# Kernel tuning notes

Measured on AMD Instinct MI355X. Metric: run time of the kernel, lower is better.

## Reference

```python
import jax, jax.numpy as jnp
import numpy as np

G = 64        # graphs per batch
N = 256       # nodes per graph (= num omics modalities)
O = 256       # omics modalities
D_IN = 128    # per-omics input dim
H = 64        # hidden_dim
HEADS = 4
E_PER = 8192  # edges per graph (avg degree 32)
NUM_NODES = G * N
E = G * E_PER
BN_EPS = 1e-5


def setup_inputs() -> dict:
    key = jax.random.key(0)
    ks = jax.random.split(key, 24)
    f = jax.random.normal
    # per-graph random edges, offset into the batched node space
    src = jax.random.randint(ks[0], (G, E_PER), 0, N)
    dst = jax.random.randint(ks[1], (G, E_PER), 0, N)
    off = (jnp.arange(G) * N)[:, None]
    edge_index = jnp.stack([(src + off).reshape(-1), (dst + off).reshape(-1)]).astype(jnp.int64)
    batch_ids = jnp.repeat(jnp.arange(G), N).astype(jnp.int64)
    return {
        "omics": f(ks[2], (G, O, D_IN), jnp.float32),
        "w_omics": f(ks[3], (O, D_IN, H), jnp.float32) * 0.05,
        "b_omics": f(ks[4], (O, H), jnp.float32) * 0.05,
        "rot": f(ks[5], (O, H), jnp.float32),
        "bn_gamma": jnp.ones((O, H), jnp.float32),
        "bn_beta": jnp.zeros((O, H), jnp.float32),
        "bn_mean": f(ks[6], (O, H), jnp.float32) * 0.1,
        "bn_var": jax.random.uniform(ks[7], (O, H), jnp.float32, 0.5, 1.5),
        "gat1_w": f(ks[8], (H, HEADS * H), jnp.float32) * 0.05,
        "att_src1": f(ks[9], (HEADS, H), jnp.float32) * 0.05,
        "att_dst1": f(ks[10], (HEADS, H), jnp.float32) * 0.05,
        "bias1": jnp.zeros((HEADS * H,), jnp.float32),
        "gat2_w": f(ks[11], (HEADS * H, H), jnp.float32) * 0.05,
        "att_src2": f(ks[12], (1, H), jnp.float32) * 0.05,
        "att_dst2": f(ks[13], (1, H), jnp.float32) * 0.05,
        "bias2": jnp.zeros((H,), jnp.float32),
        "cls_w1": f(ks[14], (H, H), jnp.float32) * 0.05,
        "cls_b1": jnp.zeros((H,), jnp.float32),
        "cls_w2": f(ks[15], (H, 1), jnp.float32) * 0.05,
        "cls_b2": jnp.zeros((1,), jnp.float32),
        "edge_index": edge_index,
        "batch_ids": batch_ids,
    }


def _gat(x, src, dst, W, a_src, a_dst, bias, heads, c):
    # PyG GATConv: linear -> per-edge attention logits -> segment softmax over dst -> scatter-sum
    h = (x @ W).reshape(-1, heads, c)                       # [NUM_NODES, heads, c]
    a_s = jnp.sum(h * a_src, axis=-1)                       # [NUM_NODES, heads]
    a_d = jnp.sum(h * a_dst, axis=-1)
    logit = jax.nn.leaky_relu(a_s[src] + a_d[dst], 0.2)     # [E, heads]
    m = jax.ops.segment_max(logit, dst, num_segments=NUM_NODES)
    m = jnp.where(jnp.isfinite(m), m, 0.0)                  # nodes with no in-edges
    e = jnp.exp(logit - m[dst])
    s = jax.ops.segment_sum(e, dst, num_segments=NUM_NODES)
    alpha = e / (s[dst] + 1e-16)                            # [E, heads]
    msg = h[src] * alpha[..., None]                         # [E, heads, c] (dominant traffic)
    out = jax.ops.segment_sum(msg, dst, num_segments=NUM_NODES)
    return out.reshape(NUM_NODES, heads * c) + bias


def reference(omics, w_omics, b_omics, rot, bn_gamma, bn_beta, bn_mean, bn_var,
              gat1_w, att_src1, att_dst1, bias1, gat2_w, att_src2, att_dst2, bias2,
              cls_w1, cls_b1, cls_w2, cls_b2, edge_index, batch_ids):
    # quantum-inspired omics encoders (vectorized over the O modalities)
    h = jnp.einsum('bod,odh->boh', omics, w_omics) + b_omics
    h = jax.nn.relu(h * (jnp.cos(rot) + jnp.sin(rot)))
    h = (h - bn_mean) / jnp.sqrt(bn_var + BN_EPS) * bn_gamma + bn_beta  # BatchNorm eval mode
    x = h.reshape(NUM_NODES, H)

    src, dst = edge_index[0], edge_index[1]
    x = jax.nn.elu(_gat(x, src, dst, gat1_w, att_src1, att_dst1, bias1, HEADS, H))
    x = _gat(x, src, dst, gat2_w, att_src2, att_dst2, bias2, 1, H)

    pooled = jax.ops.segment_sum(x, batch_ids, num_segments=G) / N  # global_mean_pool
    z = jax.nn.relu(pooled @ cls_w1 + cls_b1)
    out = jax.nn.sigmoid(z @ cls_w2 + cls_b2)
    return out, pooled
```

## Files before the change

### kernel.cpp

```cpp
#include <hip/hip_runtime.h>
#include <hip/hip_bf16.h>
#include <math.h>

#define G 64
#define NNODE 256
#define D_IN 128
#define HDIM 64
#define HEADS 4
#define E_PER 8192
#define NUM_NODES (G * NNODE)
#define E_TOTAL (G * E_PER)
#define BN_EPS 1e-5f

typedef __attribute__((ext_vector_type(8))) short bf16x8;
typedef __attribute__((ext_vector_type(4))) float f32x4;

__device__ __forceinline__ float lrelu02(float x) { return x > 0.f ? x : 0.2f * x; }
__device__ __forceinline__ unsigned short f2bf(float f) {
    unsigned u = __float_as_uint(f);
    return (unsigned short)((u + 0x7FFFu + ((u >> 16) & 1u)) >> 16);
}
__device__ __forceinline__ unsigned long long pk4(float a, float b, float c, float d) {
    return (unsigned long long)f2bf(a)
         | ((unsigned long long)f2bf(b) << 16)
         | ((unsigned long long)f2bf(c) << 32)
         | ((unsigned long long)f2bf(d) << 48);
}

__global__ __launch_bounds__(512) void setup_kernel(
    const int* __restrict__ eidx, unsigned int* __restrict__ cntm,
    const float* __restrict__ omics, const float* __restrict__ w,
    const float* __restrict__ b, const float* __restrict__ rot,
    const float* __restrict__ gamma, const float* __restrict__ beta,
    const float* __restrict__ mean, const float* __restrict__ var,
    unsigned short* __restrict__ xb,
    const float* __restrict__ w1, const float* __restrict__ w2,
    unsigned short* __restrict__ wt1, unsigned short* __restrict__ wt2)
{
    __shared__ union {
        struct { float Wl[D_IN * HDIM]; float Om[G * 132]; } enc;
        unsigned cw[NNODE * 64];
    } sm;
    int blk = blockIdx.x;
    int t = threadIdx.x;

    if (blk < G) {
        int g = blk;
        float4 z4 = make_float4(0.f, 0.f, 0.f, 0.f);
        for (int i = t; i < 4096; i += 512) ((float4*)sm.cw)[i] = z4;
        __syncthreads();
        const int* srcp = eidx + (size_t)g * E_PER;
        const int* dstp = eidx + E_TOTAL + (size_t)g * E_PER;
        int base = g * NNODE;
        for (int e = t; e < E_PER; e += 512) {
            int s = srcp[e] - base, d = dstp[e] - base;
            atomicAdd(&sm.cw[(d << 6) + (s >> 2)], 1u << ((s & 3) * 8));
        }
        __syncthreads();
        for (int i = t; i < 4096; i += 512)
            ((float4*)(cntm + (size_t)g * 16384))[i] = ((const float4*)sm.cw)[i];
    } else if (blk < G + 256) {
        int o = blk - G;
        for (int i = t; i < D_IN * HDIM / 4; i += 512)
            ((float4*)sm.enc.Wl)[i] = ((const float4*)(w + (size_t)o * D_IN * HDIM))[i];
        for (int i = t; i < G * (D_IN / 4); i += 512) {
            int g = i >> 5, dq = i & 31;
            *((float4*)(sm.enc.Om + g * 132) + dq) =
                ((const float4*)(omics + ((size_t)g * NNODE + o) * D_IN))[dq];
        }
        __syncthreads();

        int cq = t & 15, gs = t >> 4;
        float4 acc[2];
        acc[0] = make_float4(0.f, 0.f, 0.f, 0.f);
        acc[1] = make_float4(0.f, 0.f, 0.f, 0.f);

        for (int d = 0; d < D_IN; ++d) {
            float4 wv = *(const float4*)&sm.enc.Wl[d * 64 + cq * 4];
            #pragma unroll
            for (int gi = 0; gi < 2; ++gi) {
                float ov = sm.enc.Om[(gi * 32 + gs) * 132 + d];
                acc[gi].x = fmaf(ov, wv.x, acc[gi].x);
                acc[gi].y = fmaf(ov, wv.y, acc[gi].y);
                acc[gi].z = fmaf(ov, wv.z, acc[gi].z);
                acc[gi].w = fmaf(ov, wv.w, acc[gi].w);
            }
        }

        float4 bv = ((const float4*)b)[o * 16 + cq];
        float4 rv = ((const float4*)rot)[o * 16 + cq];
        float4 mv = ((const float4*)mean)[o * 16 + cq];
        float4 vv = ((const float4*)var)[o * 16 + cq];
        float4 gv = ((const float4*)gamma)[o * 16 + cq];
        float4 be = ((const float4*)beta)[o * 16 + cq];
        float4 sc, kk;
        sc.x = cosf(rv.x) + sinf(rv.x); sc.y = cosf(rv.y) + sinf(rv.y);
        sc.z = cosf(rv.z) + sinf(rv.z); sc.w = cosf(rv.w) + sinf(rv.w);
        kk.x = gv.x * rsqrtf(vv.x + BN_EPS); kk.y = gv.y * rsqrtf(vv.y + BN_EPS);
        kk.z = gv.z * rsqrtf(vv.z + BN_EPS); kk.w = gv.w * rsqrtf(vv.w + BN_EPS);

        #pragma unroll
        for (int gi = 0; gi < 2; ++gi) {
            int g = gi * 32 + gs;
            float4 v;
            v.x = fmaxf((acc[gi].x + bv.x) * sc.x, 0.f);
            v.y = fmaxf((acc[gi].y + bv.y) * sc.y, 0.f);
            v.z = fmaxf((acc[gi].z + bv.z) * sc.z, 0.f);
            v.w = fmaxf((acc[gi].w + bv.w) * sc.w, 0.f);
            v.x = (v.x - mv.x) * kk.x + be.x;
            v.y = (v.y - mv.y) * kk.y + be.y;
            v.z = (v.z - mv.z) * kk.z + be.z;
            v.w = (v.w - mv.w) * kk.w + be.w;
            *(unsigned long long*)&xb[((size_t)(g * NNODE + o)) * 64 + cq * 4] =
                pk4(v.x, v.y, v.z, v.w);
        }
    } else {
        int pb = blk - (G + 256);
        int i0 = pb * 2048 + t;
        #pragma unroll
        for (int it = 0; it < 4; ++it) {
            int i = i0 + it * 512;
            int c = i >> 6, k = i & 63;
            wt1[c * 64 + k] = f2bf(w1[k * 256 + c]);
            int c2 = i >> 8, k2 = i & 255;
            wt2[c2 * 256 + k2] = f2bf(w2[k2 * 64 + c2]);
        }
    }
}

__global__ __launch_bounds__(512) void gat1_lin_mfma(
    const unsigned short* __restrict__ xb, const unsigned short* __restrict__ wt1,
    const float* __restrict__ att_s, const float* __restrict__ att_d,
    unsigned short* __restrict__ ht1, float* __restrict__ as1, float* __restrict__ ad1)
{
    int blk = blockIdx.x;
    int n0 = blk * 64;
    int g = n0 >> 8, soff = n0 & 255;
    __shared__ unsigned short Ab[64 * 64];
    __shared__ unsigned short Bb[256 * 64];
    int t = threadIdx.x;
    {
        int node = t >> 3, kg = t & 7;
        bf16x8 v = *(const bf16x8*)&xb[(size_t)(n0 + node) * 64 + kg * 8];
        *(bf16x8*)&Ab[node * 64 + ((kg ^ (node & 7)) << 3)] = v;
    }
    for (int i = t; i < 2048; i += 512) {
        int c = i >> 3, kg = i & 7;
        bf16x8 v = *(const bf16x8*)&wt1[c * 64 + kg * 8];
        *(bf16x8*)&Bb[c * 64 + ((kg ^ (c & 7)) << 3)] = v;
    }
    __syncthreads();

    int w = t >> 6, l = t & 63;
    int lrow = l & 15, lk = l >> 4;
    int mt = w >> 1, hh0 = (w & 1) * 2;
    int arow = mt * 16 + lrow;
    float asp[2][4], adp[2][4];
    #pragma unroll
    for (int hi = 0; hi < 2; ++hi)
        #pragma unroll
        for (int r = 0; r < 4; ++r) { asp[hi][r] = 0.f; adp[hi][r] = 0.f; }

    for (int ntl = 0; ntl < 8; ++ntl) {
        int nt = (w & 1) * 8 + ntl;
        int c = nt * 16 + lrow;
        f32x4 acc = {0.f, 0.f, 0.f, 0.f};
        #pragma unroll
        for (int kb = 0; kb < 2; ++kb) {
            int kg = kb * 4 + lk;
            bf16x8 a = *(const bf16x8*)&Ab[arow * 64 + ((kg ^ (arow & 7)) << 3)];
            bf16x8 b = *(const bf16x8*)&Bb[c * 64 + ((kg ^ (c & 7)) << 3)];
            acc = __builtin_amdgcn_mfma_f32_16x16x32_bf16(a, b, acc, 0, 0, 0);
        }
        int head = c >> 6, ch = c & 63;
        int sb = soff + mt * 16 + lk * 4;
        *(unsigned long long*)&ht1[(size_t)((g * HEADS + head) * 64 + ch) * 256 + sb] =
            pk4(acc[0], acc[1], acc[2], acc[3]);
        float av = att_s[c], dv = att_d[c];
        int hi = ntl >> 2;
        #pragma unroll
        for (int r = 0; r < 4; ++r) {
            asp[hi][r] = fmaf(acc[r], av, asp[hi][r]);
            adp[hi][r] = fmaf(acc[r], dv, adp[hi][r]);
        }
    }
    #pragma unroll
    for (int hi = 0; hi < 2; ++hi)
        #pragma unroll
        for (int r = 0; r < 4; ++r) {
            float a = asp[hi][r], d = adp[hi][r];
            a += __shfl_xor(a, 1); a += __shfl_xor(a, 2);
            a += __shfl_xor(a, 4); a += __shfl_xor(a, 8);
            d += __shfl_xor(d, 1); d += __shfl_xor(d, 2);
            d += __shfl_xor(d, 4); d += __shfl_xor(d, 8);
            if (lrow == 0) {
                int node = n0 + mt * 16 + lk * 4 + r;
                as1[node * HEADS + hh0 + hi] = a;
                ad1[node * HEADS + hh0 + hi] = d;
            }
        }
}

__global__ __launch_bounds__(512) void gat1_edge_mfma(
    const unsigned short* __restrict__ ht1, const float* __restrict__ as1,
    const float* __restrict__ ad1, const unsigned int* __restrict__ cntm,
    const float* __restrict__ bias1, unsigned short* __restrict__ x2b)
{
    int g = blockIdx.x, head = blockIdx.y, q = blockIdx.z;
    __shared__ unsigned short ht[64 * 256];
    __shared__ unsigned short Mb[64 * 256];
    __shared__ float asl[NNODE], adl[NNODE], u1[NNODE], u2[NNODE];
    __shared__ float v1[NNODE], v2[NNODE];
    __shared__ float wred[8];
    unsigned short* xs = Mb;
    int t = threadIdx.x;
    int r0 = q * 64;

    float va = -1e30f, vd = 0.f;
    if (t < NNODE) {
        va = as1[(g * NNODE + t) * HEADS + head];
        vd = ad1[(g * NNODE + t) * HEADS + head];
        asl[t] = va; adl[t] = vd;
    }
    {
        float mv = va;
        #pragma unroll
        for (int d = 32; d; d >>= 1) mv = fmaxf(mv, __shfl_xor(mv, d));
        if ((t & 63) == 0) wred[t >> 6] = mv;
    }
    __syncthreads();
    if (t < NNODE) {
        float M = fmaxf(fmaxf(wred[0], wred[1]), fmaxf(wred[2], wred[3]));
        float mt = lrelu02(M + vd);
        v1[t] = __expf(vd - mt);
        v2[t] = __expf(0.2f * vd - mt);
        u1[t] = __expf(va);
        u2[t] = __expf(0.2f * va);
    }
    for (int i = t; i < 2048; i += 512) {
        int c = i >> 5, sg = i & 31;
        bf16x8 v = *(const bf16x8*)&ht1[(size_t)((g * HEADS + head) * 64 + c) * 256 + sg * 8];
        *(bf16x8*)&ht[c * 256 + ((sg ^ (c & 31)) << 3)] = v;
    }
    __syncthreads();

    int w = t >> 6, l = t & 63;
    int lrow = l & 15, lk = l >> 4;
    int mt = w & 3, nb = (w >> 2) * 2;
    int ar = mt * 16 + lrow;
    int c0 = nb * 16 + lrow, c1 = c0 + 16;
    float b0v = bias1[head * 64 + c0], b1v = bias1[head * 64 + c1];
    const bf16x8 onev = {(short)0x3F80, (short)0x3F80, (short)0x3F80, (short)0x3F80,
                         (short)0x3F80, (short)0x3F80, (short)0x3F80, (short)0x3F80};

    for (int ri = w; ri < 64; ri += 8) {
        int d = r0 + ri;
        unsigned cwv = cntm[(((size_t)g * NNODE + d) << 6) + l];
        float adv = adl[d], vd1 = v1[d], vd2 = v2[d];
        float4 as4 = ((const float4*)asl)[l];
        float4 u14 = ((const float4*)u1)[l];
        float4 u24 = ((const float4*)u2)[l];
        float p0 = (float)(cwv & 0xFFu) *
                   ((as4.x + adv > 0.f) ? u14.x * vd1 : u24.x * vd2);
        float p1 = (float)((cwv >> 8) & 0xFFu) *
                   ((as4.y + adv > 0.f) ? u14.y * vd1 : u24.y * vd2);
        float p2 = (float)((cwv >> 16) & 0xFFu) *
                   ((as4.z + adv > 0.f) ? u14.z * vd1 : u24.z * vd2);
        float p3 = (float)(cwv >> 24) *
                   ((as4.w + adv > 0.f) ? u14.w * vd1 : u24.w * vd2);
        *(unsigned long long*)&Mb[ri * 256 + (((l >> 1) ^ (ri & 7)) << 3)
                                  + ((l & 1) << 2)] = pk4(p0, p1, p2, p3);
    }
    __syncthreads();

    f32x4 acc0 = {0.f, 0.f, 0.f, 0.f};
    f32x4 acc1 = {0.f, 0.f, 0.f, 0.f};
    f32x4 accd = {0.f, 0.f, 0.f, 0.f};
    #pragma unroll
    for (int kb = 0; kb < 8; ++kb) {
        int oct = kb * 4 + lk;
        bf16x8 a = *(const bf16x8*)&Mb[ar * 256 + ((oct ^ (ar & 7)) << 3)];
        bf16x8 b0 = *(const bf16x8*)&ht[c0 * 256 + ((oct ^ (c0 & 31)) << 3)];
        bf16x8 b1 = *(const bf16x8*)&ht[c1 * 256 + ((oct ^ (c1 & 31)) << 3)];
        accd = __builtin_amdgcn_mfma_f32_16x16x32_bf16(a, onev, accd, 0, 0, 0);
        acc0 = __builtin_amdgcn_mfma_f32_16x16x32_bf16(a, b0, acc0, 0, 0, 0);
        acc1 = __builtin_amdgcn_mfma_f32_16x16x32_bf16(a, b1, acc1, 0, 0, 0);
    }
    __syncthreads();
    #pragma unroll
    for (int r = 0; r < 4; ++r) {
        int rl = mt * 16 + lk * 4 + r;
        float inv = 1.f / (accd[r] + 1e-16f);
        float o0 = acc0[r] * inv + b0v;
        float o1 = acc1[r] * inv + b1v;
        o0 = o0 > 0.f ? o0 : expm1f(o0);
        o1 = o1 > 0.f ? o1 : expm1f(o1);
        xs[rl * 64 + c0] = f2bf(o0);
        xs[rl * 64 + c1] = f2bf(o1);
    }
    __syncthreads();
    {
        int row = t >> 3, cg = t & 7;
        bf16x8 v = *(const bf16x8*)&xs[row * 64 + cg * 8];
        *(bf16x8*)&x2b[(size_t)(g * NNODE + r0 + row) * 256 + head * 64 + cg * 8] = v;
    }
}

__global__ __launch_bounds__(512) void gat2_lin_mfma(
    const unsigned short* __restrict__ x2b, const unsigned short* __restrict__ wt2,
    const float* __restrict__ att_s, const float* __restrict__ att_d,
    unsigned short* __restrict__ ht2, float* __restrict__ as2, float* __restrict__ ad2)
{
    int blk = blockIdx.x;
    int n0 = blk * 64;
    int g = n0 >> 8, soff = n0 & 255;
    __shared__ unsigned short Ab[64 * 256];
    __shared__ unsigned short Bb[64 * 256];
    __shared__ float asr[64], adr[64];
    int t = threadIdx.x;
    for (int i = t; i < 2048; i += 512) {
        int node = i >> 5, kg = i & 31;
        bf16x8 v = *(const bf16x8*)&x2b[(size_t)(n0 + node) * 256 + kg * 8];
        *(bf16x8*)&Ab[node * 256 + ((kg ^ (node & 31)) << 3)] = v;
    }
    for (int i = t; i < 2048; i += 512) {
        int c = i >> 5, kg = i & 31;
        bf16x8 v = *(const bf16x8*)&wt2[c * 256 + kg * 8];
        *(bf16x8*)&Bb[c * 256 + ((kg ^ (c & 31)) << 3)] = v;
    }
    if (t < 64) { asr[t] = 0.f; adr[t] = 0.f; }
    __syncthreads();

    int w = t >> 6, l = t & 63;
    int lrow = l & 15, lk = l >> 4;
    int mt = w & 3, nb = (w >> 2) * 2;
    int ar = mt * 16 + lrow;
    float asp[2][4], adp[2][4];
    #pragma unroll
    for (int ni = 0; ni < 2; ++ni)
        #pragma unroll
        for (int r = 0; r < 4; ++r) { asp[ni][r] = 0.f; adp[ni][r] = 0.f; }

    #pragma unroll
    for (int ni = 0; ni < 2; ++ni) {
        int c = (nb + ni) * 16 + lrow;
        f32x4 acc = {0.f, 0.f, 0.f, 0.f};
        #pragma unroll
        for (int ks = 0; ks < 8; ++ks) {
            int kg = ks * 4 + lk;
            bf16x8 a = *(const bf16x8*)&Ab[ar * 256 + ((kg ^ (ar & 31)) << 3)];
            bf16x8 b = *(const bf16x8*)&Bb[c * 256 + ((kg ^ (c & 31)) << 3)];
            acc = __builtin_amdgcn_mfma_f32_16x16x32_bf16(a, b, acc, 0, 0, 0);
        }
        int sb = soff + mt * 16 + lk * 4;
        *(unsigned long long*)&ht2[(size_t)(g * 64 + c) * 256 + sb] =
            pk4(acc[0], acc[1], acc[2], acc[3]);
        float av = att_s[c], dv = att_d[c];
        #pragma unroll
        for (int r = 0; r < 4; ++r) {
            asp[ni][r] = fmaf(acc[r], av, asp[ni][r]);
            adp[ni][r] = fmaf(acc[r], dv, adp[ni][r]);
        }
    }
    #pragma unroll
    for (int ni = 0; ni < 2; ++ni)
        #pragma unroll
        for (int r = 0; r < 4; ++r) {
            float a = asp[ni][r], d = adp[ni][r];
            a += __shfl_xor(a, 1); a += __shfl_xor(a, 2);
            a += __shfl_xor(a, 4); a += __shfl_xor(a, 8);
            d += __shfl_xor(d, 1); d += __shfl_xor(d, 2);
            d += __shfl_xor(d, 4); d += __shfl_xor(d, 8);
            if (lrow == 0) {
                int rl = mt * 16 + lk * 4 + r;
                atomicAdd(&asr[rl], a);
                atomicAdd(&adr[rl], d);
            }
        }
    __syncthreads();
    if (t < 64) { as2[n0 + t] = asr[t]; ad2[n0 + t] = adr[t]; }
}

__global__ __launch_bounds__(512) void gat2_edge_mfma(
    const unsigned short* __restrict__ ht2, const float* __restrict__ as2,
    const float* __restrict__ ad2, const unsigned int* __restrict__ cntm,
    float* __restrict__ pl8)
{
    int g = blockIdx.x, by = blockIdx.y;
    __shared__ unsigned short ht[64 * 256];
    __shared__ unsigned short Mb[32 * 256];
    __shared__ float asl[NNODE], adl[NNODE], u1[NNODE], u2[NNODE];
    __shared__ float v1[NNODE], v2[NNODE];
    __shared__ float wred[8];
    __shared__ float pool[64];
    int t = threadIdx.x;

    float va = -1e30f, vd = 0.f;
    if (t < NNODE) {
        va = as2[g * NNODE + t];
        vd = ad2[g * NNODE + t];
        asl[t] = va; adl[t] = vd;
    }
    if (t < 64) pool[t] = 0.f;
    {
        float mv = va;
        #pragma unroll
        for (int d = 32; d; d >>= 1) mv = fmaxf(mv, __shfl_xor(mv, d));
        if ((t & 63) == 0) wred[t >> 6] = mv;
    }
    __syncthreads();
    if (t < NNODE) {
        float M = fmaxf(fmaxf(wred[0], wred[1]), fmaxf(wred[2], wred[3]));
        float mt = lrelu02(M + vd);
        v1[t] = __expf(vd - mt);
        v2[t] = __expf(0.2f * vd - mt);
        u1[t] = __expf(va);
        u2[t] = __expf(0.2f * va);
    }
    for (int i = t; i < 2048; i += 512) {
        int c = i >> 5, sg = i & 31;
        bf16x8 v = *(const bf16x8*)&ht2[(size_t)(g * 64 + c) * 256 + sg * 8];
        *(bf16x8*)&ht[c * 256 + ((sg ^ (c & 31)) << 3)] = v;
    }
    __syncthreads();

    int w = t >> 6, l = t & 63;
    int lrow = l & 15, lk = l >> 4;
    int r0 = by * 32;

    for (int ri = w; ri < 32; ri += 8) {
        int d = r0 + ri;
        unsigned cwv = cntm[(((size_t)g * NNODE + d) << 6) + l];
        float adv = adl[d], vd1 = v1[d], vd2 = v2[d];
        float4 as4 = ((const float4*)asl)[l];
        float4 u14 = ((const float4*)u1)[l];
        float4 u24 = ((const float4*)u2)[l];
        float p0 = (float)(cwv & 0xFFu) *
                   ((as4.x + adv > 0.f) ? u14.x * vd1 : u24.x * vd2);
        float p1 = (float)((cwv >> 8) & 0xFFu) *
                   ((as4.y + adv > 0.f) ? u14.y * vd1 : u24.y * vd2);
        float p2 = (float)((cwv >> 16) & 0xFFu) *
                   ((as4.z + adv > 0.f) ? u14.z * vd1 : u24.z * vd2);
        float p3 = (float)(cwv >> 24) *
                   ((as4.w + adv > 0.f) ? u14.w * vd1 : u24.w * vd2);
        *(unsigned long long*)&Mb[ri * 256 + (((l >> 1) ^ (ri & 7)) << 3)
                                  + ((l & 1) << 2)] = pk4(p0, p1, p2, p3);
    }
    __syncthreads();

    const bf16x8 onev = {(short)0x3F80, (short)0x3F80, (short)0x3F80, (short)0x3F80,
                         (short)0x3F80, (short)0x3F80, (short)0x3F80, (short)0x3F80};
    int mt = w & 1, nt = w >> 1;
    f32x4 acc = {0.f, 0.f, 0.f, 0.f};
    f32x4 accd = {0.f, 0.f, 0.f, 0.f};
    int ar = mt * 16 + lrow;
    int c = nt * 16 + lrow;
    #pragma unroll
    for (int kb = 0; kb < 8; ++kb) {
        int oct = kb * 4 + lk;
        bf16x8 a = *(const bf16x8*)&Mb[ar * 256 + ((oct ^ (ar & 7)) << 3)];
        bf16x8 b = *(const bf16x8*)&ht[c * 256 + ((oct ^ (c & 31)) << 3)];
        accd = __builtin_amdgcn_mfma_f32_16x16x32_bf16(a, onev, accd, 0, 0, 0);
        acc = __builtin_amdgcn_mfma_f32_16x16x32_bf16(a, b, acc, 0, 0, 0);
    }
    float ps = 0.f;
    #pragma unroll
    for (int r = 0; r < 4; ++r)
        ps = fmaf(acc[r], 1.f / (accd[r] + 1e-16f), ps);
    ps += __shfl_xor(ps, 16);
    ps += __shfl_xor(ps, 32);
    if (l < 16) atomicAdd(&pool[nt * 16 + lrow], ps);
    __syncthreads();
    if (t < 64) pl8[(size_t)(g * 8 + by) * 64 + t] = pool[t];
}

__global__ __launch_bounds__(64) void cls_kernel(
    const float* __restrict__ pl8, const float* __restrict__ bias2,
    const float* __restrict__ w1, const float* __restrict__ b1,
    const float* __restrict__ w2, const float* __restrict__ b2,
    float* __restrict__ outv, float* __restrict__ pooled)
{
    int g = blockIdx.x, c = threadIdx.x;
    float po = 0.f;
    #pragma unroll
    for (int q = 0; q < 8; ++q) po += pl8[(size_t)(g * 8 + q) * 64 + c];
    po = po * (1.f / 256.f) + bias2[c];
    pooled[g * 64 + c] = po;
    __shared__ float poL[64];
    poL[c] = po;
    __syncthreads();
    float acc = b1[c];
    for (int k = 0; k < 64; ++k) acc = fmaf(poL[k], w1[k * 64 + c], acc);
    acc = fmaxf(acc, 0.f);
    float contrib = acc * w2[c];
    #pragma unroll
    for (int d = 32; d; d >>= 1) contrib += __shfl_xor(contrib, d);
    if (c == 0) outv[g] = 1.f / (1.f + __expf(-contrib));
}

extern "C" void kernel_launch(void* const* d_in, const int* in_sizes, int n_in,
                              void* d_out, int out_size, void* d_ws, size_t ws_size,
                              hipStream_t stream) {
    const float* omics   = (const float*)d_in[0];
    const float* w_omics = (const float*)d_in[1];
    const float* b_omics = (const float*)d_in[2];
    const float* rot     = (const float*)d_in[3];
    const float* bn_g    = (const float*)d_in[4];
    const float* bn_b    = (const float*)d_in[5];
    const float* bn_m    = (const float*)d_in[6];
    const float* bn_v    = (const float*)d_in[7];
    const float* gat1_w  = (const float*)d_in[8];
    const float* att_s1  = (const float*)d_in[9];
    const float* att_d1  = (const float*)d_in[10];
    const float* bias1   = (const float*)d_in[11];
    const float* gat2_w  = (const float*)d_in[12];
    const float* att_s2  = (const float*)d_in[13];
    const float* att_d2  = (const float*)d_in[14];
    const float* bias2   = (const float*)d_in[15];
    const float* cls_w1  = (const float*)d_in[16];
    const float* cls_b1  = (const float*)d_in[17];
    const float* cls_w2  = (const float*)d_in[18];
    const float* cls_b2  = (const float*)d_in[19];
    const int*   eidx    = (const int*)d_in[20];

    float* ws = (float*)d_ws;
    size_t o_xb   = 0;
    size_t o_ht1  = o_xb  + (size_t)NUM_NODES * 64 / 2;
    size_t o_as1  = o_ht1 + (size_t)G * HEADS * 64 * 256 / 2;
    size_t o_ad1  = o_as1 + (size_t)NUM_NODES * HEADS;
    size_t o_x2b  = o_ad1 + (size_t)NUM_NODES * HEADS;
    size_t o_ht2  = o_x2b + (size_t)NUM_NODES * 256 / 2;
    size_t o_as2  = o_ht2 + (size_t)G * 64 * 256 / 2;
    size_t o_ad2  = o_as2 + (size_t)NUM_NODES;
    size_t o_pl8  = o_ad2 + (size_t)NUM_NODES;
    size_t o_cnt  = o_pl8 + (size_t)G * 8 * 64;
    size_t o_wt1  = o_cnt + (size_t)G * 16384;
    size_t o_wt2  = o_wt1 + 8192;

    unsigned short* xb  = (unsigned short*)(ws + o_xb);
    unsigned short* ht1 = (unsigned short*)(ws + o_ht1);
    float* as1 = ws + o_as1;
    float* ad1 = ws + o_ad1;
    unsigned short* x2b = (unsigned short*)(ws + o_x2b);
    unsigned short* ht2 = (unsigned short*)(ws + o_ht2);
    float* as2 = ws + o_as2;
    float* ad2 = ws + o_ad2;
    float* pl8 = ws + o_pl8;
    unsigned int* cntm = (unsigned int*)(ws + o_cnt);
    unsigned short* wt1 = (unsigned short*)(ws + o_wt1);
    unsigned short* wt2 = (unsigned short*)(ws + o_wt2);

    float* outv   = (float*)d_out;
    float* pooled = (float*)d_out + G;

    setup_kernel<<<G + 256 + 8, 512, 0, stream>>>(
        eidx, cntm,
        omics, w_omics, b_omics, rot, bn_g, bn_b, bn_m, bn_v, xb,
        gat1_w, gat2_w, wt1, wt2);
    gat1_lin_mfma<<<256, 512, 0, stream>>>(xb, wt1, att_s1, att_d1, ht1, as1, ad1);
    gat1_edge_mfma<<<dim3(G, HEADS, 4), 512, 0, stream>>>(
        ht1, as1, ad1, cntm, bias1, x2b);
    gat2_lin_mfma<<<256, 512, 0, stream>>>(x2b, wt2, att_s2, att_d2, ht2, as2, ad2);
    gat2_edge_mfma<<<dim3(G, 8), 512, 0, stream>>>(
        ht2, as2, ad2, cntm, pl8);
    cls_kernel<<<G, 64, 0, stream>>>(pl8, bias2, cls_w1, cls_b1, cls_w2, cls_b2,
                                     outv, pooled);
}
```

Before: 62.00 us.

## Fuse GAT linear projections into edge-aggregation kernels and drop intermediate buffers

Each GAT layer's node projection and attention-logit computation now happens inside the edge aggregation kernel, writing projected features straight into shared memory instead of global buffers. This removes two kernel launches and the global write/read of projected features and attention scalars. In exchange, every block recomputes the full per-graph projection, so layer 1 repeats it across the 4 row chunks and layer 2 across the 8 row chunks, adding redundant MFMA work and global operand loads.

```diff
diff --git a/kernel.cpp b/kernel.cpp
--- a/kernel.cpp
+++ b/kernel.cpp
@@ -128,82 +128,10 @@
     }
 }
 
-__global__ __launch_bounds__(512) void gat1_lin_mfma(
+__global__ __launch_bounds__(512) void gat1_fused(
     const unsigned short* __restrict__ xb, const unsigned short* __restrict__ wt1,
+    const unsigned int* __restrict__ cntm,
     const float* __restrict__ att_s, const float* __restrict__ att_d,
-    unsigned short* __restrict__ ht1, float* __restrict__ as1, float* __restrict__ ad1)
-{
-    int blk = blockIdx.x;
-    int n0 = blk * 64;
-    int g = n0 >> 8, soff = n0 & 255;
-    __shared__ unsigned short Ab[64 * 64];
-    __shared__ unsigned short Bb[256 * 64];
-    int t = threadIdx.x;
-    {
-        int node = t >> 3, kg = t & 7;
-        bf16x8 v = *(const bf16x8*)&xb[(size_t)(n0 + node) * 64 + kg * 8];
-        *(bf16x8*)&Ab[node * 64 + ((kg ^ (node & 7)) << 3)] = v;
-    }
-    for (int i = t; i < 2048; i += 512) {
-        int c = i >> 3, kg = i & 7;
-        bf16x8 v = *(const bf16x8*)&wt1[c * 64 + kg * 8];
-        *(bf16x8*)&Bb[c * 64 + ((kg ^ (c & 7)) << 3)] = v;
-    }
-    __syncthreads();
-
-    int w = t >> 6, l = t & 63;
-    int lrow = l & 15, lk = l >> 4;
-    int mt = w >> 1, hh0 = (w & 1) * 2;
-    int arow = mt * 16 + lrow;
-    float asp[2][4], adp[2][4];
-    #pragma unroll
-    for (int hi = 0; hi < 2; ++hi)
-        #pragma unroll
-        for (int r = 0; r < 4; ++r) { asp[hi][r] = 0.f; adp[hi][r] = 0.f; }
-
-    for (int ntl = 0; ntl < 8; ++ntl) {
-        int nt = (w & 1) * 8 + ntl;
-        int c = nt * 16 + lrow;
-        f32x4 acc = {0.f, 0.f, 0.f, 0.f};
-        #pragma unroll
-        for (int kb = 0; kb < 2; ++kb) {
-            int kg = kb * 4 + lk;
-            bf16x8 a = *(const bf16x8*)&Ab[arow * 64 + ((kg ^ (arow & 7)) << 3)];
-            bf16x8 b = *(const bf16x8*)&Bb[c * 64 + ((kg ^ (c & 7)) << 3)];
-            acc = __builtin_amdgcn_mfma_f32_16x16x32_bf16(a, b, acc, 0, 0, 0);
-        }
-        int head = c >> 6, ch = c & 63;
-        int sb = soff + mt * 16 + lk * 4;
-        *(unsigned long long*)&ht1[(size_t)((g * HEADS + head) * 64 + ch) * 256 + sb] =
-            pk4(acc[0], acc[1], acc[2], acc[3]);
-        float av = att_s[c], dv = att_d[c];
-        int hi = ntl >> 2;
-        #pragma unroll
-        for (int r = 0; r < 4; ++r) {
-            asp[hi][r] = fmaf(acc[r], av, asp[hi][r]);
-            adp[hi][r] = fmaf(acc[r], dv, adp[hi][r]);
-        }
-    }
-    #pragma unroll
-    for (int hi = 0; hi < 2; ++hi)
-        #pragma unroll
-        for (int r = 0; r < 4; ++r) {
-            float a = asp[hi][r], d = adp[hi][r];
-            a += __shfl_xor(a, 1); a += __shfl_xor(a, 2);
-            a += __shfl_xor(a, 4); a += __shfl_xor(a, 8);
-            d += __shfl_xor(d, 1); d += __shfl_xor(d, 2);
-            d += __shfl_xor(d, 4); d += __shfl_xor(d, 8);
-            if (lrow == 0) {
-                int node = n0 + mt * 16 + lk * 4 + r;
-                as1[node * HEADS + hh0 + hi] = a;
-                ad1[node * HEADS + hh0 + hi] = d;
-            }
-        }
-}
-
-__global__ __launch_bounds__(512) void gat1_edge_mfma(
-    const unsigned short* __restrict__ ht1, const float* __restrict__ as1,
-    const float* __restrict__ ad1, const unsigned int* __restrict__ cntm,
     const float* __restrict__ bias1, unsigned short* __restrict__ x2b)
 {
     int g = blockIdx.x, head = blockIdx.y, q = blockIdx.z;
@@ -215,15 +143,67 @@
     unsigned short* xs = Mb;
     int t = threadIdx.x;
     int r0 = q * 64;
-
-    float va = -1e30f, vd = 0.f;
-    if (t < NNODE) {
-        va = as1[(g * NNODE + t) * HEADS + head];
-        vd = ad1[(g * NNODE + t) * HEADS + head];
-        asl[t] = va; adl[t] = vd;
-    }
+    int w = t >> 6, l = t & 63;
+    int lrow = l & 15, lk = l >> 4;
+
     {
-        float mv = va;
+        f32x4 acc[2][4];
+        #pragma unroll
+        for (int mi = 0; mi < 2; ++mi)
+            #pragma unroll
+            for (int cj = 0; cj < 4; ++cj) {
+                f32x4 z = {0.f, 0.f, 0.f, 0.f};
+                acc[mi][cj] = z;
+            }
+        #pragma unroll
+        for (int kb = 0; kb < 2; ++kb) {
+            int kslot = (kb * 4 + lk) * 8;
+            bf16x8 bfrag[4];
+            #pragma unroll
+            for (int cj = 0; cj < 4; ++cj)
+                bfrag[cj] = *(const bf16x8*)&wt1[(head * 64 + cj * 16 + lrow) * 64 + kslot];
+            #pragma unroll
+            for (int mi = 0; mi < 2; ++mi) {
+                int s = (2 * w + mi) * 16 + lrow;
+                bf16x8 a = *(const bf16x8*)&xb[(size_t)(g * NNODE + s) * 64 + kslot];
+                #pragma unroll
+                for (int cj = 0; cj < 4; ++cj)
+                    acc[mi][cj] = __builtin_amdgcn_mfma_f32_16x16x32_bf16(
+                        a, bfrag[cj], acc[mi][cj], 0, 0, 0);
+            }
+        }
+        #pragma unroll
+        for (int mi = 0; mi < 2; ++mi) {
+            int s0 = (2 * w + mi) * 16 + lk * 4;
+            float asv[4] = {0.f, 0.f, 0.f, 0.f};
+            float adv[4] = {0.f, 0.f, 0.f, 0.f};
+            #pragma unroll
+            for (int cj = 0; cj < 4; ++cj) {
+                int c = cj * 16 + lrow;
+                *(unsigned long long*)&ht[c * 256 + (((s0 >> 3) ^ (c & 31)) << 3) + (s0 & 7)] =
+                    pk4(acc[mi][cj][0], acc[mi][cj][1], acc[mi][cj][2], acc[mi][cj][3]);
+                float av = att_s[head * 64 + c], dv = att_d[head * 64 + c];
+                #pragma unroll
+                for (int r = 0; r < 4; ++r) {
+                    asv[r] = fmaf(acc[mi][cj][r], av, asv[r]);
+                    adv[r] = fmaf(acc[mi][cj][r], dv, adv[r]);
+                }
+            }
+            #pragma unroll
+            for (int r = 0; r < 4; ++r) {
+                float a = asv[r], d = adv[r];
+                a += __shfl_xor(a, 1); a += __shfl_xor(a, 2);
+                a += __shfl_xor(a, 4); a += __shfl_xor(a, 8);
+                d += __shfl_xor(d, 1); d += __shfl_xor(d, 2);
+                d += __shfl_xor(d, 4); d += __shfl_xor(d, 8);
+                if (lrow == 0) { asl[s0 + r] = a; adl[s0 + r] = d; }
+            }
+        }
+    }
+    __syncthreads();
+
+    {
+        float mv = (t < NNODE) ? asl[t] : -1e30f;
         #pragma unroll
         for (int d = 32; d; d >>= 1) mv = fmaxf(mv, __shfl_xor(mv, d));
         if ((t & 63) == 0) wred[t >> 6] = mv;
@@ -231,21 +211,15 @@
     __syncthreads();
     if (t < NNODE) {
         float M = fmaxf(fmaxf(wred[0], wred[1]), fmaxf(wred[2], wred[3]));
+        float vd = adl[t], va = asl[t];
         float mt = lrelu02(M + vd);
         v1[t] = __expf(vd - mt);
         v2[t] = __expf(0.2f * vd - mt);
         u1[t] = __expf(va);
         u2[t] = __expf(0.2f * va);
     }
-    for (int i = t; i < 2048; i += 512) {
-        int c = i >> 5, sg = i & 31;
-        bf16x8 v = *(const bf16x8*)&ht1[(size_t)((g * HEADS + head) * 64 + c) * 256 + sg * 8];
-        *(bf16x8*)&ht[c * 256 + ((sg ^ (c & 31)) << 3)] = v;
-    }
-    __syncthreads();
-
-    int w = t >> 6, l = t & 63;
-    int lrow = l & 15, lk = l >> 4;
+    __syncthreads();
+
     int mt = w & 3, nb = (w >> 2) * 2;
     int ar = mt * 16 + lrow;
     int c0 = nb * 16 + lrow, c1 = c0 + 16;
@@ -306,84 +280,10 @@
     }
 }
 
-__global__ __launch_bounds__(512) void gat2_lin_mfma(
+__global__ __launch_bounds__(512) void gat2_fused(
     const unsigned short* __restrict__ x2b, const unsigned short* __restrict__ wt2,
+    const unsigned int* __restrict__ cntm,
     const float* __restrict__ att_s, const float* __restrict__ att_d,
-    unsigned short* __restrict__ ht2, float* __restrict__ as2, float* __restrict__ ad2)
-{
-    int blk = blockIdx.x;
-    int n0 = blk * 64;
-    int g = n0 >> 8, soff = n0 & 255;
-    __shared__ unsigned short Ab[64 * 256];
-    __shared__ unsigned short Bb[64 * 256];
-    __shared__ float asr[64], adr[64];
-    int t = threadIdx.x;
-    for (int i = t; i < 2048; i += 512) {
-        int node = i >> 5, kg = i & 31;
-        bf16x8 v = *(const bf16x8*)&x2b[(size_t)(n0 + node) * 256 + kg * 8];
-        *(bf16x8*)&Ab[node * 256 + ((kg ^ (node & 31)) << 3)] = v;
-    }
-    for (int i = t; i < 2048; i += 512) {
-        int c = i >> 5, kg = i & 31;
-        bf16x8 v = *(const bf16x8*)&wt2[c * 256 + kg * 8];
-        *(bf16x8*)&Bb[c * 256 + ((kg ^ (c & 31)) << 3)] = v;
-    }
-    if (t < 64) { asr[t] = 0.f; adr[t] = 0.f; }
-    __syncthreads();
-
-    int w = t >> 6, l = t & 63;
-    int lrow = l & 15, lk = l >> 4;
-    int mt = w & 3, nb = (w >> 2) * 2;
-    int ar = mt * 16 + lrow;
-    float asp[2][4], adp[2][4];
-    #pragma unroll
-    for (int ni = 0; ni < 2; ++ni)
-        #pragma unroll
-        for (int r = 0; r < 4; ++r) { asp[ni][r] = 0.f; adp[ni][r] = 0.f; }
-
-    #pragma unroll
-    for (int ni = 0; ni < 2; ++ni) {
-        int c = (nb + ni) * 16 + lrow;
-        f32x4 acc = {0.f, 0.f, 0.f, 0.f};
-        #pragma unroll
-        for (int ks = 0; ks < 8; ++ks) {
-            int kg = ks * 4 + lk;
-            bf16x8 a = *(const bf16x8*)&Ab[ar * 256 + ((kg ^ (ar & 31)) << 3)];
-            bf16x8 b = *(const bf16x8*)&Bb[c * 256 + ((kg ^ (c & 31)) << 3)];
-            acc = __builtin_amdgcn_mfma_f32_16x16x32_bf16(a, b, acc, 0, 0, 0);
-        }
-        int sb = soff + mt * 16 + lk * 4;
-        *(unsigned long long*)&ht2[(size_t)(g * 64 + c) * 256 + sb] =
-            pk4(acc[0], acc[1], acc[2], acc[3]);
-        float av = att_s[c], dv = att_d[c];
-        #pragma unroll
-        for (int r = 0; r < 4; ++r) {
-            asp[ni][r] = fmaf(acc[r], av, asp[ni][r]);
-            adp[ni][r] = fmaf(acc[r], dv, adp[ni][r]);
-        }
-    }
-    #pragma unroll
-    for (int ni = 0; ni < 2; ++ni)
-        #pragma unroll
-        for (int r = 0; r < 4; ++r) {
-            float a = asp[ni][r], d = adp[ni][r];
-            a += __shfl_xor(a, 1); a += __shfl_xor(a, 2);
-            a += __shfl_xor(a, 4); a += __shfl_xor(a, 8);
-            d += __shfl_xor(d, 1); d += __shfl_xor(d, 2);
-            d += __shfl_xor(d, 4); d += __shfl_xor(d, 8);
-            if (lrow == 0) {
-                int rl = mt * 16 + lk * 4 + r;
-                atomicAdd(&asr[rl], a);
-                atomicAdd(&adr[rl], d);
-            }
-        }
-    __syncthreads();
-    if (t < 64) { as2[n0 + t] = asr[t]; ad2[n0 + t] = adr[t]; }
-}
-
-__global__ __launch_bounds__(512) void gat2_edge_mfma(
-    const unsigned short* __restrict__ ht2, const float* __restrict__ as2,
-    const float* __restrict__ ad2, const unsigned int* __restrict__ cntm,
     float* __restrict__ pl8)
 {
     int g = blockIdx.x, by = blockIdx.y;
@@ -394,16 +294,68 @@
     __shared__ float wred[8];
     __shared__ float pool[64];
     int t = threadIdx.x;
-
-    float va = -1e30f, vd = 0.f;
-    if (t < NNODE) {
-        va = as2[g * NNODE + t];
-        vd = ad2[g * NNODE + t];
-        asl[t] = va; adl[t] = vd;
-    }
+    int w = t >> 6, l = t & 63;
+    int lrow = l & 15, lk = l >> 4;
+    int r0 = by * 32;
     if (t < 64) pool[t] = 0.f;
+
     {
-        float mv = va;
+        f32x4 acc[2][4];
+        #pragma unroll
+        for (int mi = 0; mi < 2; ++mi)
+            #pragma unroll
+            for (int cj = 0; cj < 4; ++cj) {
+                f32x4 z = {0.f, 0.f, 0.f, 0.f};
+                acc[mi][cj] = z;
+            }
+        for (int kb = 0; kb < 8; ++kb) {
+            int kslot = (kb * 4 + lk) * 8;
+            bf16x8 bfrag[4];
+            #pragma unroll
+            for (int cj = 0; cj < 4; ++cj)
+                bfrag[cj] = *(const bf16x8*)&wt2[(cj * 16 + lrow) * 256 + kslot];
+            #pragma unroll
+            for (int mi = 0; mi < 2; ++mi) {
+                int s = (2 * w + mi) * 16 + lrow;
+                bf16x8 a = *(const bf16x8*)&x2b[(size_t)(g * NNODE + s) * 256 + kslot];
+                #pragma unroll
+                for (int cj = 0; cj < 4; ++cj)
+                    acc[mi][cj] = __builtin_amdgcn_mfma_f32_16x16x32_bf16(
+                        a, bfrag[cj], acc[mi][cj], 0, 0, 0);
+            }
+        }
+        #pragma unroll
+        for (int mi = 0; mi < 2; ++mi) {
+            int s0 = (2 * w + mi) * 16 + lk * 4;
+            float asv[4] = {0.f, 0.f, 0.f, 0.f};
+            float adv[4] = {0.f, 0.f, 0.f, 0.f};
+            #pragma unroll
+            for (int cj = 0; cj < 4; ++cj) {
+                int c = cj * 16 + lrow;
+                *(unsigned long long*)&ht[c * 256 + (((s0 >> 3) ^ (c & 31)) << 3) + (s0 & 7)] =
+                    pk4(acc[mi][cj][0], acc[mi][cj][1], acc[mi][cj][2], acc[mi][cj][3]);
+                float av = att_s[c], dv = att_d[c];
+                #pragma unroll
+                for (int r = 0; r < 4; ++r) {
+                    asv[r] = fmaf(acc[mi][cj][r], av, asv[r]);
+                    adv[r] = fmaf(acc[mi][cj][r], dv, adv[r]);
+                }
+            }
+            #pragma unroll
+            for (int r = 0; r < 4; ++r) {
+                float a = asv[r], d = adv[r];
+                a += __shfl_xor(a, 1); a += __shfl_xor(a, 2);
+                a += __shfl_xor(a, 4); a += __shfl_xor(a, 8);
+                d += __shfl_xor(d, 1); d += __shfl_xor(d, 2);
+                d += __shfl_xor(d, 4); d += __shfl_xor(d, 8);
+                if (lrow == 0) { asl[s0 + r] = a; adl[s0 + r] = d; }
+            }
+        }
+    }
+    __syncthreads();
+
+    {
+        float mv = (t < NNODE) ? asl[t] : -1e30f;
         #pragma unroll
         for (int d = 32; d; d >>= 1) mv = fmaxf(mv, __shfl_xor(mv, d));
         if ((t & 63) == 0) wred[t >> 6] = mv;
@@ -411,22 +363,14 @@
     __syncthreads();
     if (t < NNODE) {
         float M = fmaxf(fmaxf(wred[0], wred[1]), fmaxf(wred[2], wred[3]));
+        float vd = adl[t], va = asl[t];
         float mt = lrelu02(M + vd);
         v1[t] = __expf(vd - mt);
         v2[t] = __expf(0.2f * vd - mt);
         u1[t] = __expf(va);
         u2[t] = __expf(0.2f * va);
     }
-    for (int i = t; i < 2048; i += 512) {
-        int c = i >> 5, sg = i & 31;
-        bf16x8 v = *(const bf16x8*)&ht2[(size_t)(g * 64 + c) * 256 + sg * 8];
-        *(bf16x8*)&ht[c * 256 + ((sg ^ (c & 31)) << 3)] = v;
-    }
-    __syncthreads();
-
-    int w = t >> 6, l = t & 63;
-    int lrow = l & 15, lk = l >> 4;
-    int r0 = by * 32;
+    __syncthreads();
 
     for (int ri = w; ri < 32; ri += 8) {
         int d = r0 + ri;
@@ -525,26 +469,14 @@
 
     float* ws = (float*)d_ws;
     size_t o_xb   = 0;
-    size_t o_ht1  = o_xb  + (size_t)NUM_NODES * 64 / 2;
-    size_t o_as1  = o_ht1 + (size_t)G * HEADS * 64 * 256 / 2;
-    size_t o_ad1  = o_as1 + (size_t)NUM_NODES * HEADS;
-    size_t o_x2b  = o_ad1 + (size_t)NUM_NODES * HEADS;
-    size_t o_ht2  = o_x2b + (size_t)NUM_NODES * 256 / 2;
-    size_t o_as2  = o_ht2 + (size_t)G * 64 * 256 / 2;
-    size_t o_ad2  = o_as2 + (size_t)NUM_NODES;
-    size_t o_pl8  = o_ad2 + (size_t)NUM_NODES;
+    size_t o_x2b  = o_xb  + (size_t)NUM_NODES * 64 / 2;
+    size_t o_pl8  = o_x2b + (size_t)NUM_NODES * 256 / 2;
     size_t o_cnt  = o_pl8 + (size_t)G * 8 * 64;
     size_t o_wt1  = o_cnt + (size_t)G * 16384;
     size_t o_wt2  = o_wt1 + 8192;
 
     unsigned short* xb  = (unsigned short*)(ws + o_xb);
-    unsigned short* ht1 = (unsigned short*)(ws + o_ht1);
-    float* as1 = ws + o_as1;
-    float* ad1 = ws + o_ad1;
     unsigned short* x2b = (unsigned short*)(ws + o_x2b);
-    unsigned short* ht2 = (unsigned short*)(ws + o_ht2);
-    float* as2 = ws + o_as2;
-    float* ad2 = ws + o_ad2;
     float* pl8 = ws + o_pl8;
     unsigned int* cntm = (unsigned int*)(ws + o_cnt);
     unsigned short* wt1 = (unsigned short*)(ws + o_wt1);
@@ -557,12 +489,10 @@
         eidx, cntm,
         omics, w_omics, b_omics, rot, bn_g, bn_b, bn_m, bn_v, xb,
         gat1_w, gat2_w, wt1, wt2);
-    gat1_lin_mfma<<<256, 512, 0, stream>>>(xb, wt1, att_s1, att_d1, ht1, as1, ad1);
-    gat1_edge_mfma<<<dim3(G, HEADS, 4), 512, 0, stream>>>(
-        ht1, as1, ad1, cntm, bias1, x2b);
-    gat2_lin_mfma<<<256, 512, 0, stream>>>(x2b, wt2, att_s2, att_d2, ht2, as2, ad2);
-    gat2_edge_mfma<<<dim3(G, 8), 512, 0, stream>>>(
-        ht2, as2, ad2, cntm, pl8);
+    gat1_fused<<<dim3(G, HEADS, 4), 512, 0, stream>>>(
+        xb, wt1, cntm, att_s1, att_d1, bias1, x2b);
+    gat2_fused<<<dim3(G, 8), 512, 0, stream>>>(
+        x2b, wt2, cntm, att_s2, att_d2, pl8);
     cls_kernel<<<G, 64, 0, stream>>>(pl8, bias2, cls_w1, cls_b1, cls_w2, cls_b2,
                                      outv, pooled);
 }
```

New measurement: 82.82 us. 33.6% more time.
